# Performance work log

Measured on AMD Instinct MI355X. Metric: run time of the kernel, lower is better.

Reference implementation:

```python
import jax, jax.numpy as jnp
import numpy as np

# Ordered bi-bi mechanism, species order per _build_species_list:
# [E, EA, EQ, EAB, A, B, P, Q] -> indices 0..7
# Transitions: E+A<->EA, EA+B<->EAB, EAB<->EQ+P, EQ<->E+Q (all reversible)
N_SPECIES = 8
N_TRANS = 4

# forward: rate * [enzyme] * prod([substrates]); -1 = no factor (padded)
ENZ_F = np.array([0, 1, 3, 2], dtype=np.int32)          # E, EA, EAB, EQ
SUB_F = np.array([[4], [5], [-1], [-1]], dtype=np.int32)  # A, B, -, -
# reverse: rate * [to-enzyme] * prod([products])
ENZ_R = np.array([1, 3, 2, 0], dtype=np.int32)          # EA, EAB, EQ, E
PROD_R = np.array([[-1], [-1], [6], [7]], dtype=np.int32)  # -, -, P, Q
REV_MASK = np.array([1.0, 1.0, 1.0, 1.0], dtype=np.float32)

# Stoichiometry (n_trans, n_species), applied as dydt += v_net[:,None]*S[i]
S_FORWARD = np.array([
    [-1,  1,  0,  0, -1,  0,  0,  0],
    [ 0, -1,  0,  1,  0, -1,  0,  0],
    [ 0,  0,  1, -1,  0,  0,  1,  0],
    [ 1,  0, -1,  0,  0,  0,  0,  1],
], dtype=np.float32)


def _masked_gather_prod(y, idx):
    # y: (B, n_species); idx: (n_trans, k) with -1 padding
    safe = jnp.maximum(idx, 0)
    g = y[:, safe.reshape(-1)].reshape(y.shape[0], idx.shape[0], idx.shape[1])  # (B,T,k)
    g = jnp.where(idx[None, :, :] >= 0, g, 1.0)
    return jnp.prod(g, axis=-1)  # (B, T)


def setup_inputs() -> dict:
    key = jax.random.key(0)
    k1, k2, k3 = jax.random.split(key, 3)
    B = 2_000_000
    return {
        "t": jnp.zeros((1,), dtype=jnp.float32),
        "y": jax.random.uniform(k1, (B, N_SPECIES), dtype=jnp.float32),
        "forward_rates": jax.random.uniform(k2, (B, N_TRANS), dtype=jnp.float32),
        "reverse_rates": jax.random.uniform(k3, (B, N_TRANS), dtype=jnp.float32),
    }


def reference(t, y, forward_rates, reverse_rates):
    enz_f = jnp.asarray(ENZ_F)
    enz_r = jnp.asarray(ENZ_R)
    sub_f = jnp.asarray(SUB_F)
    prod_r = jnp.asarray(PROD_R)
    S = jnp.asarray(S_FORWARD)
    rev_mask = jnp.asarray(REV_MASK)

    # v_forward[b,i] = k_f[b,i] * y[b, enz_f[i]] * prod_j y[b, sub_f[i,j]]
    v_f = forward_rates * y[:, enz_f] * _masked_gather_prod(y, sub_f)
    # v_reverse analogous, zeroed for irreversible transitions
    v_r = reverse_rates * y[:, enz_r] * _masked_gather_prod(y, prod_r) * rev_mask[None, :]
    v_net = v_f - v_r  # (B, T)
    # dydt[b,s] = sum_i v_net[b,i] * S[i,s]
    return jnp.einsum("bt,ts->bs", v_net, S)
```

## Files before the change

kernel.cpp:

```cpp
#include <hip/hip_runtime.h>


__global__ __launch_bounds__(256) void ode_kernel(
    const float* __restrict__ y,
    const float* __restrict__ kf,
    const float* __restrict__ kr,
    float* __restrict__ out,
    int B)
{
    int i = blockIdx.x * blockDim.x + threadIdx.x;
    if (i >= B) return;

    const float4* y4 = reinterpret_cast<const float4*>(y) + (size_t)i * 2;
    float4 ya = y4[0];
    float4 yb = y4[1];
    float4 f  = reinterpret_cast<const float4*>(kf)[i];
    float4 r  = reinterpret_cast<const float4*>(kr)[i];

    float E   = ya.x, EA = ya.y, EQ = ya.z, EAB = ya.w;
    float A   = yb.x, Bc = yb.y, P  = yb.z, Q   = yb.w;

    float v0 = f.x * E   * A  - r.x * EA;
    float v1 = f.y * EA  * Bc - r.y * EAB;
    float v2 = f.z * EAB      - r.z * EQ * P;
    float v3 = f.w * EQ       - r.w * E  * Q;

    float4 o0, o1;
    o0.x = v3 - v0;
    o0.y = v0 - v1;
    o0.z = v2 - v3;
    o0.w = v1 - v2;
    o1.x = -v0;
    o1.y = -v1;
    o1.z =  v2;
    o1.w =  v3;

    float4* out4 = reinterpret_cast<float4*>(out) + (size_t)i * 2;
    out4[0] = o0;
    out4[1] = o1;
}

extern "C" void kernel_launch(void* const* d_in, const int* in_sizes, int n_in,
                              void* d_out, int out_size, void* d_ws, size_t ws_size,
                              hipStream_t stream) {
    const float* y  = (const float*)d_in[1];
    const float* kf = (const float*)d_in[2];
    const float* kr = (const float*)d_in[3];
    float* out = (float*)d_out;
    int B = in_sizes[1] / 8;

    int block = 256;
    int grid = (B + block - 1) / block;
    ode_kernel<<<grid, block, 0, stream>>>(y, kf, kr, out, B);
}
```

Measured before the change: 169.0 us.

## Split each batch element across two lanes with shuffle exchange for contiguous accesses

Each element is now handled by two threads. Each thread loads one float4 of y (adjacent lanes cover a contiguous 32-byte row) and either the forward or reverse rate vector, then swaps the halves with __shfl_xor. The goal is fully contiguous wavefront-wide loads and stores instead of the previous two-float4 strided per-thread pattern, and twice as many threads in flight for a memory-bound kernel. In exchange it adds cross-lane shuffles, a divergent pointer select, and duplicated arithmetic across each lane pair.

After: 168.2 us. No clear change (-0.5%).

```diff
diff --git a/kernel.cpp b/kernel.cpp
--- a/kernel.cpp
+++ b/kernel.cpp
@@ -2,54 +2,75 @@
 
 
 __global__ __launch_bounds__(256) void ode_kernel(
-    const float* __restrict__ y,
-    const float* __restrict__ kf,
-    const float* __restrict__ kr,
-    float* __restrict__ out,
-    int B)
+    const float4* __restrict__ y4,
+    const float4* __restrict__ kf4,
+    const float4* __restrict__ kr4,
+    float4* __restrict__ out4,
+    int n2)
 {
-    int i = blockIdx.x * blockDim.x + threadIdx.x;
-    if (i >= B) return;
+    int t = blockIdx.x * blockDim.x + threadIdx.x;
+    if (t >= n2) return;
 
-    const float4* y4 = reinterpret_cast<const float4*>(y) + (size_t)i * 2;
-    float4 ya = y4[0];
-    float4 yb = y4[1];
-    float4 f  = reinterpret_cast<const float4*>(kf)[i];
-    float4 r  = reinterpret_cast<const float4*>(kr)[i];
+    int e = t >> 1;
+    int h = t & 1;
 
-    float E   = ya.x, EA = ya.y, EQ = ya.z, EAB = ya.w;
-    float A   = yb.x, Bc = yb.y, P  = yb.z, Q   = yb.w;
+    float4 q = y4[t];
+
+    float4 p;
+    p.x = __shfl_xor(q.x, 1);
+    p.y = __shfl_xor(q.y, 1);
+    p.z = __shfl_xor(q.z, 1);
+    p.w = __shfl_xor(q.w, 1);
+
+    float4 ya = h ? p : q;
+    float4 yb = h ? q : p;
+
+    const float4* __restrict__ rp = h ? kr4 : kf4;
+    float4 mine = rp[e];
+    float4 other;
+    other.x = __shfl_xor(mine.x, 1);
+    other.y = __shfl_xor(mine.y, 1);
+    other.z = __shfl_xor(mine.z, 1);
+    other.w = __shfl_xor(mine.w, 1);
+
+    float4 f = h ? other : mine;
+    float4 r = h ? mine : other;
+
+    float E  = ya.x, EA = ya.y, EQ = ya.z, EAB = ya.w;
+    float A  = yb.x, Bc = yb.y, P  = yb.z, Q   = yb.w;
 
     float v0 = f.x * E   * A  - r.x * EA;
     float v1 = f.y * EA  * Bc - r.y * EAB;
     float v2 = f.z * EAB      - r.z * EQ * P;
     float v3 = f.w * EQ       - r.w * E  * Q;
 
-    float4 o0, o1;
-    o0.x = v3 - v0;
-    o0.y = v0 - v1;
-    o0.z = v2 - v3;
-    o0.w = v1 - v2;
-    o1.x = -v0;
-    o1.y = -v1;
-    o1.z =  v2;
-    o1.w =  v3;
+    float4 o;
+    if (h == 0) {
+        o.x = v3 - v0;
+        o.y = v0 - v1;
+        o.z = v2 - v3;
+        o.w = v1 - v2;
+    } else {
+        o.x = -v0;
+        o.y = -v1;
+        o.z =  v2;
+        o.w =  v3;
+    }
 
-    float4* out4 = reinterpret_cast<float4*>(out) + (size_t)i * 2;
-    out4[0] = o0;
-    out4[1] = o1;
+    out4[t] = o;
 }
 
 extern "C" void kernel_launch(void* const* d_in, const int* in_sizes, int n_in,
                               void* d_out, int out_size, void* d_ws, size_t ws_size,
                               hipStream_t stream) {
-    const float* y  = (const float*)d_in[1];
-    const float* kf = (const float*)d_in[2];
-    const float* kr = (const float*)d_in[3];
-    float* out = (float*)d_out;
-    int B = in_sizes[1] / 8;
+    const float4* y4  = (const float4*)d_in[1];
+    const float4* kf4 = (const float4*)d_in[2];
+    const float4* kr4 = (const float4*)d_in[3];
+    float4* out4 = (float4*)d_out;
+    int B  = in_sizes[1] / 8;
+    int n2 = 2 * B;
 
     int block = 256;
-    int grid = (B + block - 1) / block;
-    ode_kernel<<<grid, block, 0, stream>>>(y, kf, kr, out, B);
+    int grid = (n2 + block - 1) / block;
+    ode_kernel<<<grid, block, 0, stream>>>(y4, kf4, kr4, out4, n2);
 }
```
